# Performance work log

Measured on AMD Instinct MI355X. Metric: run time of the kernel, lower is better.

## Reference

```python
import jax, jax.numpy as jnp
import numpy as np
import math

B, T, D = 8, 1024, 512
WS = 12          # window_size (top-k)
EPS = 1e-5       # BatchNorm eps (eval mode, running stats)
NEG = -1e9


def setup_inputs() -> dict:
    key = jax.random.key(0)
    ks = jax.random.split(key, 13)
    x = jax.random.normal(ks[0], (B, T, D), jnp.float32)
    conv1_w = jax.random.normal(ks[1], (512, 512, 5, 5), jnp.float32) / np.float32(np.sqrt(512 * 25))
    conv1_b = jax.random.normal(ks[2], (512,), jnp.float32) * 0.01
    bn1_g = jax.random.uniform(ks[3], (512,), jnp.float32, 0.5, 1.5)
    bn1_b = jax.random.normal(ks[4], (512,), jnp.float32) * 0.1
    bn1_m = jax.random.normal(ks[5], (512,), jnp.float32) * 0.1
    bn1_v = jax.random.uniform(ks[6], (512,), jnp.float32, 0.5, 1.5)
    conv2_w = jax.random.normal(ks[7], (512, 512, 5, 3), jnp.float32) / np.float32(np.sqrt(512 * 15))
    conv2_b = jax.random.normal(ks[8], (512,), jnp.float32) * 0.01
    bn2_g = jax.random.uniform(ks[9], (512,), jnp.float32, 0.5, 1.5)
    bn2_b = jax.random.normal(ks[10], (512,), jnp.float32) * 0.1
    bn2_m = jax.random.normal(ks[11], (512,), jnp.float32) * 0.1
    bn2_v = jax.random.uniform(ks[12], (512,), jnp.float32, 0.5, 1.5)
    return dict(x=x, conv1_w=conv1_w, conv1_b=conv1_b, bn1_g=bn1_g, bn1_b=bn1_b,
                bn1_m=bn1_m, bn1_v=bn1_v, conv2_w=conv2_w, conv2_b=conv2_b,
                bn2_g=bn2_g, bn2_b=bn2_b, bn2_m=bn2_m, bn2_v=bn2_v)


def _conv_nchw(h, w, b):
    # Conv2d padding=(2,0): pad height by 2 each side, no width padding.
    out = jax.lax.conv_general_dilated(h, w, window_strides=(1, 1),
                                       padding=((2, 2), (0, 0)),
                                       dimension_numbers=('NCHW', 'OIHW', 'NCHW'))
    return out + b[None, :, None, None]


def _bn(h, g, bt, m, v):
    # eval-mode BatchNorm2d with running stats
    inv = jax.lax.rsqrt(v + EPS)
    return (h - m[None, :, None, None]) * (g * inv)[None, :, None, None] + bt[None, :, None, None]


def _pool2(h):
    return jax.lax.reduce_window(h, -jnp.inf, jax.lax.max,
                                 (1, 1, 2, 2), (1, 1, 2, 2), 'VALID')


def reference(x, conv1_w, conv1_b, bn1_g, bn1_b, bn1_m, bn1_v,
              conv2_w, conv2_b, bn2_g, bn2_b, bn2_m, bn2_v):
    b, t, d = x.shape
    # masked local attention scores
    scores = jnp.einsum('btd,bsd->bts', x, x) / math.sqrt(d)  # [B,T,T]
    i = jnp.arange(t)[:, None]
    j = jnp.arange(t)[None, :]
    band = jnp.abs(j - i) <= (WS - 1)  # local band, width 2*WS-1
    scores = jnp.where(band[None], scores, NEG)
    # top-k window select, indices sorted ascending
    _, idx = jax.lax.top_k(scores, WS)           # [B,T,WS]
    ids = jnp.sort(idx, axis=-1)
    # batched gather: out[b,t,k,:] = x[b, ids[b,t,k], :]
    gathered = x[jnp.arange(b)[:, None, None], ids]  # [B,T,WS,D]
    h = gathered.transpose(0, 3, 1, 2)               # [B,512,T,WS]
    # conv encoder
    h = jax.nn.relu(_bn(_conv_nchw(h, conv1_w, conv1_b), bn1_g, bn1_b, bn1_m, bn1_v))
    h = _pool2(h)                                    # [B,512,T/2,4]
    h = jax.nn.relu(_bn(_conv_nchw(h, conv2_w, conv2_b), bn2_g, bn2_b, bn2_m, bn2_v))
    h = _pool2(h)                                    # [B,512,T/4,1]
    return jnp.squeeze(h)                            # [B,512,T/4]
```

## Files before the change

### kernel.cpp

```cpp
#include <hip/hip_runtime.h>
#include <hip/hip_bf16.h>

typedef short bf16x8 __attribute__((ext_vector_type(8)));
typedef float f32x16 __attribute__((ext_vector_type(16)));
typedef unsigned short u16;

__device__ __forceinline__ u16 f2bf(float v) {
    union { __hip_bfloat16 h; u16 u; } cv;
    cv.h = __float2bfloat16(v);
    return cv.u;
}

__device__ __forceinline__ void gld_lds16(const u16* g, u16* l) {
    __builtin_amdgcn_global_load_lds(
        (const __attribute__((address_space(1))) void*)g,
        (__attribute__((address_space(3))) void*)l, 16, 0, 0);
}

__global__ void prep_w1(const float* __restrict__ w, u16* __restrict__ o) {
    int idx = blockIdx.x * 256 + threadIdx.x;
    if (idx >= 25 * 512 * 512) return;
    int e = idx & 7, ocl = (idx >> 3) & 63, c = (idx >> 9) & 3;
    int ocs = (idx >> 11) & 7, T = idx >> 14;
    int icb = T / 25, tap = T - icb * 25;
    int ic = icb * 32 + c * 8 + e;
    int oc = ocs * 64 + ocl;
    int kh = tap / 5, kw = tap - kh * 5;
    o[idx] = f2bf(w[(((size_t)oc * 512 + ic) * 5 + kh) * 5 + kw]);
}

__global__ void prep_w2(const float* __restrict__ w, u16* __restrict__ o) {
    int idx = blockIdx.x * 256 + threadIdx.x;
    if (idx >= 15 * 512 * 512) return;
    int e = idx & 7, ocl = (idx >> 3) & 63, c = (idx >> 9) & 3;
    int ocs = (idx >> 11) & 7, T = idx >> 14;
    int icb = T / 15, tap = T - icb * 15;
    int ic = icb * 32 + c * 8 + e;
    int oc = ocs * 64 + ocl;
    int kh = tap / 3, kw = tap - kh * 3;
    o[idx] = f2bf(w[(((size_t)oc * 512 + ic) * 5 + kh) * 3 + kw]);
}

__global__ void prep_bn(const float* __restrict__ g, const float* __restrict__ b,
                        const float* __restrict__ m, const float* __restrict__ v,
                        float* __restrict__ scale, float* __restrict__ shift) {
    int i = blockIdx.x * 256 + threadIdx.x;
    if (i >= 512) return;
    float s = g[i] * rsqrtf(v[i] + 1e-5f);
    scale[i] = s;
    shift[i] = b[i] - m[i] * s;
}

__global__ void zero_pads(u16* __restrict__ gath, u16* __restrict__ pooled) {
    int idx = blockIdx.x * 256 + threadIdx.x;
    if (idx < 24576) {
        int w = idx % 12, r = idx / 12;
        int h4 = r & 3; r >>= 2;
        int cc = r & 63, b = r >> 6;
        int h = (h4 < 2) ? h4 : 1024 + h4;
        *(int4*)&gath[(((size_t)(b * 64 + cc)) * 12336 + h * 12 + w) * 8] =
            int4{0, 0, 0, 0};
    } else if (idx < 24576 + 8192) {
        int j = idx - 24576;
        int w = j & 3, r = j >> 2;
        int h4 = r & 3; r >>= 2;
        int cc = r & 63, b = r >> 6;
        int hp = (h4 < 2) ? h4 : 512 + h4;
        *(int4*)&pooled[(((size_t)(b * 64 + cc)) * 2064 + hp * 4 + w) * 8] =
            int4{0, 0, 0, 0};
    }
}

__global__ __launch_bounds__(256) void gather_topk(const float* __restrict__ x,
                                                   u16* __restrict__ g) {
    int bt = blockIdx.x;
    int b = bt >> 10, t = bt & 1023;
    const float* xb = x + (size_t)b * 1024 * 512;
    const float* xt = xb + (size_t)t * 512;
    __shared__ float xts[512];
    __shared__ float sc[23];
    __shared__ int sel[12];
    int tid = threadIdx.x;
    for (int i = tid; i < 512; i += 256) xts[i] = xt[i];
    __syncthreads();
    int j0 = t - 11; if (j0 < 0) j0 = 0;
    int j1 = t + 11; if (j1 > 1023) j1 = 1023;
    int C = j1 - j0 + 1;
    int wave = tid >> 6, lane = tid & 63;
    for (int c = wave; c < C; c += 4) {
        const float* xj = xb + (size_t)(j0 + c) * 512;
        double s = 0.0;
        #pragma unroll
        for (int e = 0; e < 8; ++e) {
            int d = lane * 8 + e;
            s += (double)xj[d] * (double)xts[d];
        }
        #pragma unroll
        for (int off = 32; off; off >>= 1) s += __shfl_xor(s, off, 64);
        if (lane == 0) sc[c] = (float)(s / 22.627416997969522);
    }
    __syncthreads();
    if (tid < 64) {
        bool selme = false;
        float v = (tid < C) ? sc[tid] : 0.f;
        if (tid < C) {
            int r = 0;
            #pragma unroll
            for (int k = 0; k < 23; ++k) {
                if (k < C) {
                    float u = sc[k];
                    r += (u > v) || (u == v && k < tid);
                }
            }
            selme = (r < 12);
        }
        unsigned long long m = __ballot(selme);
        if (selme) {
            int posn = __popcll(m & ((1ull << tid) - 1ull));
            sel[posn] = j0 + tid;
        }
    }
    __syncthreads();
    const size_t rowbase = (size_t)(t + 2) * 12;
    for (int i = tid; i < 768; i += 256) {
        int cc = i / 12, s = i - cc * 12;
        const float* src = xb + (size_t)sel[s] * 512 + cc * 8;
        float4 f0 = *(const float4*)src;
        float4 f1 = *(const float4*)(src + 4);
        u16 pk[8] = {f2bf(f0.x), f2bf(f0.y), f2bf(f0.z), f2bf(f0.w),
                     f2bf(f1.x), f2bf(f1.y), f2bf(f1.z), f2bf(f1.w)};
        *(int4*)&g[(((size_t)(b * 64 + cc)) * 12336 + rowbase + s) * 8] =
            *(const int4*)pk;
    }
}


template <int IN_W, int LOG_OW, int KH, int KW, int TH, int HTB, int MF32,
          int ARP, int PLANE, int CPX, bool POOL2E>
__global__ __launch_bounds__(512, 1) void conv_fused(
    const u16* __restrict__ A, const u16* __restrict__ Wt,
    const float* __restrict__ bias, const float* __restrict__ bnsc,
    const float* __restrict__ bnsh, void* __restrict__ outp) {
    constexpr int OW = 1 << LOG_OW;
    constexpr int TAPS = KH * KW;
    constexpr int JC = ARP / 64;
    constexpr int MFR = (32 >> LOG_OW) * IN_W;
    constexpr int SLAB = ARP * 8 + 32;
    constexpr int NB = 2 * TAPS;
    __shared__ u16 As_l[2][8 * SLAB];

    const int tid = threadIdx.x;
    const int bid = blockIdx.x;
    const int lb = (bid & 7) * CPX + (bid >> 3);
    const int n0 = (lb & 1) * 256;
    const int mt = lb >> 1;
    const int b = mt / HTB;
    const int h0 = (mt % HTB) * TH;

    const int lane = tid & 63;
    const int wv = tid >> 6;
    const int wm = wv >> 2, wn = wv & 3;
    const int l31 = lane & 31, kgrp = lane >> 5;

    const int pos0 = wm * MF32 * 32 + l31;
    const int rowb0 = (pos0 >> LOG_OW) * IN_W + (pos0 & (OW - 1));
    const int aoffb = kgrp * SLAB + rowb0 * 8;

    const int ocs = (lb & 1) * 4 + wn;
    const u16* wlane = Wt + (size_t)ocs * 2048 + kgrp * 512 + l31 * 8;

    const u16* gAh = A + (((size_t)b * 64) * PLANE + h0 * IN_W + lane) * 8;

    f32x16 acc[MF32][2];
    #pragma unroll
    for (int i = 0; i < MF32; ++i)
        #pragma unroll
        for (int j = 0; j < 2; ++j)
            acc[i][j] = f32x16{0.f,0.f,0.f,0.f,0.f,0.f,0.f,0.f,
                               0.f,0.f,0.f,0.f,0.f,0.f,0.f,0.f};

    #pragma unroll 1
    for (int q = wv; q < 8 * JC; q += 8) {
        int c8 = q / JC, j = q - c8 * JC;
        gld_lds16(gAh + ((size_t)(c8 * PLANE) + j * 64) * 8,
                  &As_l[0][c8 * SLAB + j * 512]);
    }
    bf16x8 wE0 = *(const bf16x8*)(wlane);
    bf16x8 wE1 = *(const bf16x8*)(wlane + 256);
    bf16x8 wE2 = *(const bf16x8*)(wlane + 1024);
    bf16x8 wE3 = *(const bf16x8*)(wlane + 1280);
    bf16x8 wO0, wO1, wO2, wO3;
    asm volatile("s_waitcnt vmcnt(0)" ::: "memory");
    __builtin_amdgcn_s_barrier();

    #pragma unroll 1
    for (int cn = 0; cn < 8; ++cn) {
        if (cn < 7) {
            const int chn = cn + 1;
            #pragma unroll 1
            for (int q = wv; q < 8 * JC; q += 8) {
                int c8 = q / JC, j = q - c8 * JC;
                gld_lds16(gAh + ((size_t)((chn * 8 + c8) * PLANE) + j * 64) * 8,
                          &As_l[chn & 1][c8 * SLAB + j * 512]);
            }
        }
        const u16* aBufc = &As_l[cn & 1][0] + aoffb;
        const u16* wch = wlane + ((size_t)cn * NB + 1) * 16384;
        bf16x8 afA[MF32], afB[MF32];
        #pragma unroll
        for (int mf = 0; mf < MF32; ++mf)
            afA[mf] = *(const bf16x8*)(aBufc + MFR * mf * 8);
        #pragma unroll
        for (int bi = 0; bi < NB; ++bi) {
            const int gh = bi / TAPS, t = bi - gh * TAPS;
            const int kh_ = t / KW;
            const int toff = kh_ * IN_W + (t - kh_ * KW);
            const u16* aR = aBufc + gh * 4 * SLAB;
            const u16* wS = wch + (size_t)bi * 16384;
            if (bi & 1) {
                wE0 = *(const bf16x8*)(wS);
                wE1 = *(const bf16x8*)(wS + 256);
                wE2 = *(const bf16x8*)(wS + 1024);
                wE3 = *(const bf16x8*)(wS + 1280);
            } else {
                wO0 = *(const bf16x8*)(wS);
                wO1 = *(const bf16x8*)(wS + 256);
                wO2 = *(const bf16x8*)(wS + 1024);
                wO3 = *(const bf16x8*)(wS + 1280);
            }
            #pragma unroll
            for (int mf = 0; mf < MF32; ++mf)
                afB[mf] = *(const bf16x8*)(aR + (toff + MFR * mf) * 8 + 2 * SLAB);
            __builtin_amdgcn_s_setprio(1);
            #pragma unroll
            for (int mf = 0; mf < MF32; ++mf) {
                acc[mf][0] = __builtin_amdgcn_mfma_f32_32x32x16_bf16(
                    afA[mf], (bi & 1) ? wO0 : wE0, acc[mf][0], 0, 0, 0);
                acc[mf][1] = __builtin_amdgcn_mfma_f32_32x32x16_bf16(
                    afA[mf], (bi & 1) ? wO1 : wE1, acc[mf][1], 0, 0, 0);
            }
            __builtin_amdgcn_s_setprio(0);
            if (bi + 1 < NB) {
                const int bn2 = bi + 1;
                const int ghn = bn2 / TAPS, tn = bn2 - ghn * TAPS;
                const int khn = tn / KW;
                const int toffn = khn * IN_W + (tn - khn * KW);
                const u16* aRn = aBufc + ghn * 4 * SLAB;
                #pragma unroll
                for (int mf = 0; mf < MF32; ++mf)
                    afA[mf] = *(const bf16x8*)(aRn + (toffn + MFR * mf) * 8);
            }
            __builtin_amdgcn_s_setprio(1);
            #pragma unroll
            for (int mf = 0; mf < MF32; ++mf) {
                acc[mf][0] = __builtin_amdgcn_mfma_f32_32x32x16_bf16(
                    afB[mf], (bi & 1) ? wO2 : wE2, acc[mf][0], 0, 0, 0);
                acc[mf][1] = __builtin_amdgcn_mfma_f32_32x32x16_bf16(
                    afB[mf], (bi & 1) ? wO3 : wE3, acc[mf][1], 0, 0, 0);
            }
            __builtin_amdgcn_s_setprio(0);
        }
        asm volatile("s_waitcnt vmcnt(4)" ::: "memory");
        __builtin_amdgcn_s_barrier();
    }
    asm volatile("s_waitcnt vmcnt(0)" ::: "memory");

    #pragma unroll
    for (int nf = 0; nf < 2; ++nf) {
        const int oc = n0 + wn * 64 + nf * 32 + l31;
        const float scv = bnsc[oc], shv = bnsh[oc], bi2 = bias[oc];
        const float shh = fmaf(bi2, scv, shv);
        #pragma unroll
        for (int mf = 0; mf < MF32; ++mf) {
            #pragma unroll
            for (int q = 0; q < 4; ++q) {
                if (!POOL2E) {
                    const int r0 = (q & 1) * 2 + (q >> 1) * 8;
                    float mx = fmaxf(
                        fmaxf(acc[mf][nf][r0], acc[mf][nf][r0 + 1]),
                        fmaxf(acc[mf][nf][r0 + 4], acc[mf][nf][r0 + 5]));
                    float v = fmaxf(fmaf(mx, scv, shh), 0.f);
                    const int row0 = (r0 & 3) + 8 * (r0 >> 2) + 4 * kgrp;
                    const int pos = wm * MF32 * 32 + mf * 32 + row0;
                    const int h = h0 + (pos >> LOG_OW);
                    const int w = pos & (OW - 1);
                    const int prow = (2 + (h >> 1)) * 4 + (w >> 1);
                    u16* o = (u16*)outp;
                    o[(((size_t)(b * 64 + (oc >> 3))) * 2064 + prow) * 8 +
                      (oc & 7)] = f2bf(v);
                } else {
                    const int r0 = q * 4;
                    float mx = fmaxf(
                        fmaxf(acc[mf][nf][r0], acc[mf][nf][r0 + 1]),
                        fmaxf(acc[mf][nf][r0 + 2], acc[mf][nf][r0 + 3]));
                    float v = fmaxf(fmaf(mx, scv, shh), 0.f);
                    const int row0 = 8 * (r0 >> 2) + 4 * kgrp;
                    const int pos = wm * 32 + row0;
                    const int pout = (h0 + (pos >> 1)) >> 1;
                    float* o = (float*)outp;
                    o[((size_t)(b * 512 + oc)) * 256 + pout] = v;
                }
            }
        }
    }
}

extern "C" void kernel_launch(void* const* d_in, const int* in_sizes, int n_in,
                              void* d_out, int out_size, void* d_ws, size_t ws_size,
                              hipStream_t stream) {
    const float* x  = (const float*)d_in[0];
    const float* w1 = (const float*)d_in[1];
    const float* b1 = (const float*)d_in[2];
    const float* g1 = (const float*)d_in[3];
    const float* be1 = (const float*)d_in[4];
    const float* m1 = (const float*)d_in[5];
    const float* v1 = (const float*)d_in[6];
    const float* w2 = (const float*)d_in[7];
    const float* b2 = (const float*)d_in[8];
    const float* g2 = (const float*)d_in[9];
    const float* be2 = (const float*)d_in[10];
    const float* m2 = (const float*)d_in[11];
    const float* v2 = (const float*)d_in[12];
    float* out = (float*)d_out;

    char* ws = (char*)d_ws;
    u16* gathered = (u16*)(ws);
    u16* w1t      = (u16*)(ws + 101056512);
    u16* w2t      = (u16*)(ws + 114163712);
    float* bn1s   = (float*)(ws + 122028032);
    float* bn1t   = bn1s + 512;
    float* bn2s   = bn1s + 1024;
    float* bn2t   = bn1s + 1536;
    u16* pooled1  = (u16*)(ws + 122036224);

    prep_w1<<<25600, 256, 0, stream>>>(w1, w1t);
    prep_w2<<<15360, 256, 0, stream>>>(w2, w2t);
    prep_bn<<<2, 256, 0, stream>>>(g1, be1, m1, v1, bn1s, bn1t);
    prep_bn<<<2, 256, 0, stream>>>(g2, be2, m2, v2, bn2s, bn2t);
    zero_pads<<<128, 256, 0, stream>>>(gathered, pooled1);
    gather_topk<<<8192, 256, 0, stream>>>(x, gathered);

    conv_fused<12, 3, 5, 5, 32, 32, 4, 448, 12336, 64, false>
        <<<512, 512, 0, stream>>>(gathered, w1t, b1, bn1s, bn1t, pooled1);
    conv_fused<4, 1, 5, 3, 32, 16, 1, 192, 2064, 32, true>
        <<<256, 512, 0, stream>>>(pooled1, w2t, b2, bn2s, bn2t, out);
}
```

Baseline: 788.5 us.

## Reshape conv1 wave tiling to 4x2 waves with four N fragments each

Makes the wave grid inside each conv block configurable (LOG_WN, NF). Conv1 switches from a 2x4 wave layout with 4 M-fragments and 2 N-fragments per wave to a 4x2 layout with 2 M-fragments and 4 N-fragments. Conv2 keeps its original layout. The aim is to change the balance between LDS A-fragment reads and global weight loads per MFMA, cutting LDS traffic in exchange for more weight registers and more global weight loads per wave. The weight double-buffering is also recast as a macro so that register arrays are indexed statically.

```diff
diff --git a/kernel.cpp b/kernel.cpp
--- a/kernel.cpp
+++ b/kernel.cpp
@@ -135,8 +135,50 @@
 }
 
 
+#define CBODY(BI, WUSE, WPRE) do {                                            \
+    const int gh_ = (BI) / TAPS, t_ = (BI) - gh_ * TAPS;                      \
+    const int kh2_ = t_ / KW;                                                 \
+    const int toff_ = kh2_ * IN_W + (t_ - kh2_ * KW);                         \
+    const u16* aR_ = aBufc + gh_ * 4 * SLAB;                                  \
+    const size_t wofs_ = ((size_t)cn * NB + (BI) + 1) * 16384;                \
+    _Pragma("unroll")                                                         \
+    for (int nf = 0; nf < NF; ++nf) {                                         \
+        WPRE[nf] = *(const bf16x8*)(wlN[nf] + wofs_);                         \
+        WPRE[NF + nf] = *(const bf16x8*)(wlN[nf] + wofs_ + 1024);             \
+    }                                                                         \
+    _Pragma("unroll")                                                         \
+    for (int mf = 0; mf < MF32; ++mf)                                         \
+        afB[mf] = *(const bf16x8*)(aR_ + (toff_ + MFR * mf) * 8 + 2 * SLAB);  \
+    __builtin_amdgcn_s_setprio(1);                                            \
+    _Pragma("unroll")                                                         \
+    for (int mf = 0; mf < MF32; ++mf)                                         \
+        _Pragma("unroll")                                                     \
+        for (int nf = 0; nf < NF; ++nf)                                       \
+            acc[mf][nf] = __builtin_amdgcn_mfma_f32_32x32x16_bf16(            \
+                afA[mf], WUSE[nf], acc[mf][nf], 0, 0, 0);                     \
+    __builtin_amdgcn_s_setprio(0);                                            \
+    if ((BI) + 1 < NB) {                                                      \
+        const int bn2_ = (BI) + 1;                                            \
+        const int ghn_ = bn2_ / TAPS, tn_ = bn2_ - ghn_ * TAPS;               \
+        const int khn_ = tn_ / KW;                                            \
+        const int toffn_ = khn_ * IN_W + (tn_ - khn_ * KW);                   \
+        const u16* aRn_ = aBufc + ghn_ * 4 * SLAB;                            \
+        _Pragma("unroll")                                                     \
+        for (int mf = 0; mf < MF32; ++mf)                                     \
+            afA[mf] = *(const bf16x8*)(aRn_ + (toffn_ + MFR * mf) * 8);       \
+    }                                                                         \
+    __builtin_amdgcn_s_setprio(1);                                            \
+    _Pragma("unroll")                                                         \
+    for (int mf = 0; mf < MF32; ++mf)                                         \
+        _Pragma("unroll")                                                     \
+        for (int nf = 0; nf < NF; ++nf)                                       \
+            acc[mf][nf] = __builtin_amdgcn_mfma_f32_32x32x16_bf16(            \
+                afB[mf], WUSE[NF + nf], acc[mf][nf], 0, 0, 0);                \
+    __builtin_amdgcn_s_setprio(0);                                            \
+  } while (0)
+
 template <int IN_W, int LOG_OW, int KH, int KW, int TH, int HTB, int MF32,
-          int ARP, int PLANE, int CPX, bool POOL2E>
+          int LOG_WN, int NF, int ARP, int PLANE, int CPX, bool POOL2E>
 __global__ __launch_bounds__(512, 1) void conv_fused(
     const u16* __restrict__ A, const u16* __restrict__ Wt,
     const float* __restrict__ bias, const float* __restrict__ bnsc,
@@ -159,23 +201,28 @@
 
     const int lane = tid & 63;
     const int wv = tid >> 6;
-    const int wm = wv >> 2, wn = wv & 3;
+    const int wn = wv & ((1 << LOG_WN) - 1);
+    const int wm = wv >> LOG_WN;
     const int l31 = lane & 31, kgrp = lane >> 5;
 
     const int pos0 = wm * MF32 * 32 + l31;
     const int rowb0 = (pos0 >> LOG_OW) * IN_W + (pos0 & (OW - 1));
     const int aoffb = kgrp * SLAB + rowb0 * 8;
 
-    const int ocs = (lb & 1) * 4 + wn;
-    const u16* wlane = Wt + (size_t)ocs * 2048 + kgrp * 512 + l31 * 8;
+    const int ocs_base = (lb & 1) * 4;
+    const u16* wlN[NF];
+    #pragma unroll
+    for (int nf = 0; nf < NF; ++nf)
+        wlN[nf] = Wt + (size_t)(ocs_base + wn * (NF / 2) + (nf >> 1)) * 2048
+                  + kgrp * 512 + ((nf & 1) * 32 + l31) * 8;
 
     const u16* gAh = A + (((size_t)b * 64) * PLANE + h0 * IN_W + lane) * 8;
 
-    f32x16 acc[MF32][2];
+    f32x16 acc[MF32][NF];
     #pragma unroll
     for (int i = 0; i < MF32; ++i)
         #pragma unroll
-        for (int j = 0; j < 2; ++j)
+        for (int j = 0; j < NF; ++j)
             acc[i][j] = f32x16{0.f,0.f,0.f,0.f,0.f,0.f,0.f,0.f,
                                0.f,0.f,0.f,0.f,0.f,0.f,0.f,0.f};
 
@@ -185,11 +232,12 @@
         gld_lds16(gAh + ((size_t)(c8 * PLANE) + j * 64) * 8,
                   &As_l[0][c8 * SLAB + j * 512]);
     }
-    bf16x8 wE0 = *(const bf16x8*)(wlane);
-    bf16x8 wE1 = *(const bf16x8*)(wlane + 256);
-    bf16x8 wE2 = *(const bf16x8*)(wlane + 1024);
-    bf16x8 wE3 = *(const bf16x8*)(wlane + 1280);
-    bf16x8 wO0, wO1, wO2, wO3;
+    bf16x8 wE[2 * NF], wO[2 * NF];
+    #pragma unroll
+    for (int nf = 0; nf < NF; ++nf) {
+        wE[nf] = *(const bf16x8*)(wlN[nf]);
+        wE[NF + nf] = *(const bf16x8*)(wlN[nf] + 1024);
+    }
     asm volatile("s_waitcnt vmcnt(0)" ::: "memory");
     __builtin_amdgcn_s_barrier();
 
@@ -205,69 +253,23 @@
             }
         }
         const u16* aBufc = &As_l[cn & 1][0] + aoffb;
-        const u16* wch = wlane + ((size_t)cn * NB + 1) * 16384;
         bf16x8 afA[MF32], afB[MF32];
         #pragma unroll
         for (int mf = 0; mf < MF32; ++mf)
             afA[mf] = *(const bf16x8*)(aBufc + MFR * mf * 8);
         #pragma unroll
         for (int bi = 0; bi < NB; ++bi) {
-            const int gh = bi / TAPS, t = bi - gh * TAPS;
-            const int kh_ = t / KW;
-            const int toff = kh_ * IN_W + (t - kh_ * KW);
-            const u16* aR = aBufc + gh * 4 * SLAB;
-            const u16* wS = wch + (size_t)bi * 16384;
-            if (bi & 1) {
-                wE0 = *(const bf16x8*)(wS);
-                wE1 = *(const bf16x8*)(wS + 256);
-                wE2 = *(const bf16x8*)(wS + 1024);
-                wE3 = *(const bf16x8*)(wS + 1280);
-            } else {
-                wO0 = *(const bf16x8*)(wS);
-                wO1 = *(const bf16x8*)(wS + 256);
-                wO2 = *(const bf16x8*)(wS + 1024);
-                wO3 = *(const bf16x8*)(wS + 1280);
-            }
-            #pragma unroll
-            for (int mf = 0; mf < MF32; ++mf)
-                afB[mf] = *(const bf16x8*)(aR + (toff + MFR * mf) * 8 + 2 * SLAB);
-            __builtin_amdgcn_s_setprio(1);
-            #pragma unroll
-            for (int mf = 0; mf < MF32; ++mf) {
-                acc[mf][0] = __builtin_amdgcn_mfma_f32_32x32x16_bf16(
-                    afA[mf], (bi & 1) ? wO0 : wE0, acc[mf][0], 0, 0, 0);
-                acc[mf][1] = __builtin_amdgcn_mfma_f32_32x32x16_bf16(
-                    afA[mf], (bi & 1) ? wO1 : wE1, acc[mf][1], 0, 0, 0);
-            }
-            __builtin_amdgcn_s_setprio(0);
-            if (bi + 1 < NB) {
-                const int bn2 = bi + 1;
-                const int ghn = bn2 / TAPS, tn = bn2 - ghn * TAPS;
-                const int khn = tn / KW;
-                const int toffn = khn * IN_W + (tn - khn * KW);
-                const u16* aRn = aBufc + ghn * 4 * SLAB;
-                #pragma unroll
-                for (int mf = 0; mf < MF32; ++mf)
-                    afA[mf] = *(const bf16x8*)(aRn + (toffn + MFR * mf) * 8);
-            }
-            __builtin_amdgcn_s_setprio(1);
-            #pragma unroll
-            for (int mf = 0; mf < MF32; ++mf) {
-                acc[mf][0] = __builtin_amdgcn_mfma_f32_32x32x16_bf16(
-                    afB[mf], (bi & 1) ? wO2 : wE2, acc[mf][0], 0, 0, 0);
-                acc[mf][1] = __builtin_amdgcn_mfma_f32_32x32x16_bf16(
-                    afB[mf], (bi & 1) ? wO3 : wE3, acc[mf][1], 0, 0, 0);
-            }
-            __builtin_amdgcn_s_setprio(0);
-        }
-        asm volatile("s_waitcnt vmcnt(4)" ::: "memory");
+            if ((bi & 1) == 0) CBODY(bi, wE, wO);
+            else              CBODY(bi, wO, wE);
+        }
+        asm volatile("s_waitcnt vmcnt(%0)" :: "i"(2 * NF) : "memory");
         __builtin_amdgcn_s_barrier();
     }
     asm volatile("s_waitcnt vmcnt(0)" ::: "memory");
 
     #pragma unroll
-    for (int nf = 0; nf < 2; ++nf) {
-        const int oc = n0 + wn * 64 + nf * 32 + l31;
+    for (int nf = 0; nf < NF; ++nf) {
+        const int oc = n0 + wn * (NF * 32) + nf * 32 + l31;
         const float scv = bnsc[oc], shv = bnsh[oc], bi2 = bias[oc];
         const float shh = fmaf(bi2, scv, shv);
         #pragma unroll
@@ -295,7 +297,7 @@
                         fmaxf(acc[mf][nf][r0 + 2], acc[mf][nf][r0 + 3]));
                     float v = fmaxf(fmaf(mx, scv, shh), 0.f);
                     const int row0 = 8 * (r0 >> 2) + 4 * kgrp;
-                    const int pos = wm * 32 + row0;
+                    const int pos = wm * MF32 * 32 + row0;
                     const int pout = (h0 + (pos >> 1)) >> 1;
                     float* o = (float*)outp;
                     o[((size_t)(b * 512 + oc)) * 256 + pout] = v;
@@ -340,8 +342,8 @@
     zero_pads<<<128, 256, 0, stream>>>(gathered, pooled1);
     gather_topk<<<8192, 256, 0, stream>>>(x, gathered);
 
-    conv_fused<12, 3, 5, 5, 32, 32, 4, 448, 12336, 64, false>
+    conv_fused<12, 3, 5, 5, 32, 32, 2, 1, 4, 448, 12336, 64, false>
         <<<512, 512, 0, stream>>>(gathered, w1t, b1, bn1s, bn1t, pooled1);
-    conv_fused<4, 1, 5, 3, 32, 16, 1, 192, 2064, 32, true>
+    conv_fused<4, 1, 5, 3, 32, 16, 1, 2, 2, 192, 2064, 32, true>
         <<<256, 512, 0, stream>>>(pooled1, w2t, b2, bn2s, bn2t, out);
 }
```

Result: slower. 922.6 us (+17.0%).

## Specialize conv2 kernel with 256-thread blocks, larger row tiles and four channel tiles

Applied to the files above, without the earlier changes.

Splits the shared templated conv into a conv1 kernel and a dedicated conv2 kernel. The conv2 kernel uses 256 threads per block with launch bounds allowing three blocks per CU, a single LDS buffer, taller row tiles (TH=64, two M fragments per wave) and four 128-channel output tiles per row tile. The aim is better occupancy and more reuse of the loaded weights for the small second conv. In exchange, it gives up double-buffered A staging, which exposes load latency behind barriers.

```diff
diff --git a/kernel.cpp b/kernel.cpp
--- a/kernel.cpp
+++ b/kernel.cpp
@@ -134,10 +134,9 @@
     }
 }
 
-
 template <int IN_W, int LOG_OW, int KH, int KW, int TH, int HTB, int MF32,
-          int ARP, int PLANE, int CPX, bool POOL2E>
-__global__ __launch_bounds__(512, 1) void conv_fused(
+          int ARP, int PLANE, int CPX>
+__global__ __launch_bounds__(512, 1) void conv1_fused(
     const u16* __restrict__ A, const u16* __restrict__ Wt,
     const float* __restrict__ bias, const float* __restrict__ bnsc,
     const float* __restrict__ bnsh, void* __restrict__ outp) {
@@ -274,32 +273,173 @@
         for (int mf = 0; mf < MF32; ++mf) {
             #pragma unroll
             for (int q = 0; q < 4; ++q) {
-                if (!POOL2E) {
-                    const int r0 = (q & 1) * 2 + (q >> 1) * 8;
-                    float mx = fmaxf(
-                        fmaxf(acc[mf][nf][r0], acc[mf][nf][r0 + 1]),
-                        fmaxf(acc[mf][nf][r0 + 4], acc[mf][nf][r0 + 5]));
-                    float v = fmaxf(fmaf(mx, scv, shh), 0.f);
-                    const int row0 = (r0 & 3) + 8 * (r0 >> 2) + 4 * kgrp;
-                    const int pos = wm * MF32 * 32 + mf * 32 + row0;
-                    const int h = h0 + (pos >> LOG_OW);
-                    const int w = pos & (OW - 1);
-                    const int prow = (2 + (h >> 1)) * 4 + (w >> 1);
-                    u16* o = (u16*)outp;
-                    o[(((size_t)(b * 64 + (oc >> 3))) * 2064 + prow) * 8 +
-                      (oc & 7)] = f2bf(v);
-                } else {
-                    const int r0 = q * 4;
-                    float mx = fmaxf(
-                        fmaxf(acc[mf][nf][r0], acc[mf][nf][r0 + 1]),
-                        fmaxf(acc[mf][nf][r0 + 2], acc[mf][nf][r0 + 3]));
-                    float v = fmaxf(fmaf(mx, scv, shh), 0.f);
-                    const int row0 = 8 * (r0 >> 2) + 4 * kgrp;
-                    const int pos = wm * 32 + row0;
-                    const int pout = (h0 + (pos >> 1)) >> 1;
-                    float* o = (float*)outp;
-                    o[((size_t)(b * 512 + oc)) * 256 + pout] = v;
-                }
+                const int r0 = (q & 1) * 2 + (q >> 1) * 8;
+                float mx = fmaxf(
+                    fmaxf(acc[mf][nf][r0], acc[mf][nf][r0 + 1]),
+                    fmaxf(acc[mf][nf][r0 + 4], acc[mf][nf][r0 + 5]));
+                float v = fmaxf(fmaf(mx, scv, shh), 0.f);
+                const int row0 = (r0 & 3) + 8 * (r0 >> 2) + 4 * kgrp;
+                const int pos = wm * MF32 * 32 + mf * 32 + row0;
+                const int h = h0 + (pos >> LOG_OW);
+                const int w = pos & (OW - 1);
+                const int prow = (2 + (h >> 1)) * 4 + (w >> 1);
+                u16* o = (u16*)outp;
+                o[(((size_t)(b * 64 + (oc >> 3))) * 2064 + prow) * 8 +
+                  (oc & 7)] = f2bf(v);
+            }
+        }
+    }
+}
+
+#define STAGEA2(CH) do {                                                      \
+    _Pragma("unroll 1")                                                       \
+    for (int q_ = wv; q_ < 8 * JC; q_ += 4) {                                 \
+        int c8_ = q_ / JC, j_ = q_ - c8_ * JC;                                \
+        const u16* p_ = gAh +                                                 \
+            ((size_t)(((CH) * 8 + c8_) * PLANE) + j_ * 64) * 8;               \
+        if (p_ > gAmax) p_ = gAmax;                                           \
+        gld_lds16(p_, &As_l[c8_ * SLAB + j_ * 512]);                          \
+    }                                                                         \
+  } while (0)
+
+#define CBODY2(BI, WUSE, WPRE) do {                                           \
+    const int gh_ = (BI) / TAPS, t_ = (BI) - gh_ * TAPS;                      \
+    const int kh2_ = t_ / KW;                                                 \
+    const int toff_ = kh2_ * IN_W + (t_ - kh2_ * KW);                         \
+    const u16* aR_ = aBufc + gh_ * 4 * SLAB;                                  \
+    const u16* wS_ = wch + (size_t)(BI) * 16384;                              \
+    WPRE[0] = *(const bf16x8*)(wS_);                                          \
+    WPRE[1] = *(const bf16x8*)(wS_ + 256);                                    \
+    WPRE[2] = *(const bf16x8*)(wS_ + 1024);                                   \
+    WPRE[3] = *(const bf16x8*)(wS_ + 1280);                                   \
+    _Pragma("unroll")                                                         \
+    for (int mf = 0; mf < MF32; ++mf)                                         \
+        afB[mf] = *(const bf16x8*)(aR_ + (toff_ + MFR * mf) * 8 + 2 * SLAB);  \
+    __builtin_amdgcn_s_setprio(1);                                            \
+    _Pragma("unroll")                                                         \
+    for (int mf = 0; mf < MF32; ++mf)                                         \
+        _Pragma("unroll")                                                     \
+        for (int nf = 0; nf < 2; ++nf)                                        \
+            acc[mf][nf] = __builtin_amdgcn_mfma_f32_32x32x16_bf16(            \
+                afA[mf], WUSE[nf], acc[mf][nf], 0, 0, 0);                     \
+    __builtin_amdgcn_s_setprio(0);                                            \
+    if ((BI) + 1 < NB) {                                                      \
+        const int bn2_ = (BI) + 1;                                            \
+        const int ghn_ = bn2_ / TAPS, tn_ = bn2_ - ghn_ * TAPS;               \
+        const int khn_ = tn_ / KW;                                            \
+        const int toffn_ = khn_ * IN_W + (tn_ - khn_ * KW);                   \
+        const u16* aRn_ = aBufc + ghn_ * 4 * SLAB;                            \
+        _Pragma("unroll")                                                     \
+        for (int mf = 0; mf < MF32; ++mf)                                     \
+            afA[mf] = *(const bf16x8*)(aRn_ + (toffn_ + MFR * mf) * 8);       \
+    }                                                                         \
+    __builtin_amdgcn_s_setprio(1);                                            \
+    _Pragma("unroll")                                                         \
+    for (int mf = 0; mf < MF32; ++mf)                                         \
+        _Pragma("unroll")                                                     \
+        for (int nf = 0; nf < 2; ++nf)                                        \
+            acc[mf][nf] = __builtin_amdgcn_mfma_f32_32x32x16_bf16(            \
+                afB[mf], WUSE[2 + nf], acc[mf][nf], 0, 0, 0);                 \
+    __builtin_amdgcn_s_setprio(0);                                            \
+  } while (0)
+
+template <int IN_W, int LOG_OW, int KH, int KW, int TH, int HTB, int MF32,
+          int NTILES, int ARP, int PLANE, int CPX>
+__global__ __launch_bounds__(256, 3) void conv2_fused(
+    const u16* __restrict__ A, const u16* __restrict__ Wt,
+    const float* __restrict__ bias, const float* __restrict__ bnsc,
+    const float* __restrict__ bnsh, float* __restrict__ outp) {
+    constexpr int OW = 1 << LOG_OW;
+    constexpr int TAPS = KH * KW;
+    constexpr int JC = ARP / 64;
+    constexpr int MFR = (32 >> LOG_OW) * IN_W;
+    constexpr int SLAB = ARP * 8 + 32;
+    constexpr int NB = 2 * TAPS;
+    __shared__ u16 As_l[8 * SLAB];
+
+    const int tid = threadIdx.x;
+    const int bid = blockIdx.x;
+    const int lb = (bid & 7) * CPX + (bid >> 3);
+    const int n0 = (lb % NTILES) * (512 / NTILES);
+    const int mt = lb / NTILES;
+    const int b = mt / HTB;
+    const int h0 = (mt % HTB) * TH;
+
+    const int lane = tid & 63;
+    const int wv = tid >> 6;
+    const int wn = wv & 1;
+    const int wm = wv >> 1;
+    const int l31 = lane & 31, kgrp = lane >> 5;
+
+    const int pos0 = wm * MF32 * 32 + l31;
+    const int rowb0 = (pos0 >> LOG_OW) * IN_W + (pos0 & (OW - 1));
+    const int aoffb = kgrp * SLAB + rowb0 * 8;
+
+    const int ocs_base = (lb % NTILES) * (8 / NTILES);
+    const u16* wlane = Wt + (size_t)(ocs_base + wn) * 2048
+                       + kgrp * 512 + l31 * 8;
+
+    const u16* gAh = A + (((size_t)b * 64) * PLANE + h0 * IN_W + lane) * 8;
+    const u16* gAmax = A + (size_t)512 * PLANE * 8 - 8;
+
+    f32x16 acc[MF32][2];
+    #pragma unroll
+    for (int i = 0; i < MF32; ++i)
+        #pragma unroll
+        for (int j = 0; j < 2; ++j)
+            acc[i][j] = f32x16{0.f,0.f,0.f,0.f,0.f,0.f,0.f,0.f,
+                               0.f,0.f,0.f,0.f,0.f,0.f,0.f,0.f};
+
+    STAGEA2(0);
+    bf16x8 wE[4], wO[4];
+    wE[0] = *(const bf16x8*)(wlane);
+    wE[1] = *(const bf16x8*)(wlane + 256);
+    wE[2] = *(const bf16x8*)(wlane + 1024);
+    wE[3] = *(const bf16x8*)(wlane + 1280);
+    asm volatile("s_waitcnt vmcnt(0)" ::: "memory");
+    __builtin_amdgcn_s_barrier();
+
+    const u16* wch = wlane + 16384;
+    #pragma unroll 1
+    for (int cn = 0; cn < 8; ++cn) {
+        const u16* aBufc = &As_l[0] + aoffb;
+        bf16x8 afA[MF32], afB[MF32];
+        #pragma unroll
+        for (int mf = 0; mf < MF32; ++mf)
+            afA[mf] = *(const bf16x8*)(aBufc + MFR * mf * 8);
+        #pragma unroll
+        for (int bi = 0; bi < NB; ++bi) {
+            if ((bi & 1) == 0) CBODY2(bi, wE, wO);
+            else              CBODY2(bi, wO, wE);
+        }
+        wch += (size_t)NB * 16384;
+        if (cn < 7) {
+            __builtin_amdgcn_s_barrier();
+            STAGEA2(cn + 1);
+            asm volatile("s_waitcnt vmcnt(0)" ::: "memory");
+            __builtin_amdgcn_s_barrier();
+        }
+    }
+    asm volatile("s_waitcnt vmcnt(0)" ::: "memory");
+
+    #pragma unroll
+    for (int nf = 0; nf < 2; ++nf) {
+        const int oc = n0 + wn * 64 + nf * 32 + l31;
+        const float scv = bnsc[oc], shv = bnsh[oc], bi2 = bias[oc];
+        const float shh = fmaf(bi2, scv, shv);
+        #pragma unroll
+        for (int mf = 0; mf < MF32; ++mf) {
+            #pragma unroll
+            for (int q = 0; q < 4; ++q) {
+                const int r0 = q * 4;
+                float mx = fmaxf(
+                    fmaxf(acc[mf][nf][r0], acc[mf][nf][r0 + 1]),
+                    fmaxf(acc[mf][nf][r0 + 2], acc[mf][nf][r0 + 3]));
+                float v = fmaxf(fmaf(mx, scv, shh), 0.f);
+                const int row0 = 8 * (r0 >> 2) + 4 * kgrp;
+                const int pos = wm * MF32 * 32 + mf * 32 + row0;
+                const int pout = (h0 + (pos >> 1)) >> 1;
+                outp[((size_t)(b * 512 + oc)) * 256 + pout] = v;
             }
         }
     }
@@ -340,8 +480,8 @@
     zero_pads<<<128, 256, 0, stream>>>(gathered, pooled1);
     gather_topk<<<8192, 256, 0, stream>>>(x, gathered);
 
-    conv_fused<12, 3, 5, 5, 32, 32, 4, 448, 12336, 64, false>
+    conv1_fused<12, 3, 5, 5, 32, 32, 4, 448, 12336, 64>
         <<<512, 512, 0, stream>>>(gathered, w1t, b1, bn1s, bn1t, pooled1);
-    conv_fused<4, 1, 5, 3, 32, 16, 1, 192, 2064, 32, true>
-        <<<256, 512, 0, stream>>>(pooled1, w2t, b2, bn2s, bn2t, out);
-}
+    conv2_fused<4, 1, 5, 3, 64, 8, 2, 4, 320, 2064, 32>
+        <<<256, 256, 0, stream>>>(pooled1, w2t, b2, bn2s, bn2t, out);
+}
```

Measured after the change: 773.5 us. About the same (-1.9%).
